# Performance work log

Measured on AMD Instinct MI355X. Metric: run time of the kernel, lower is better.

## Reference

```python
import jax, jax.numpy as jnp
import numpy as np
import math

SR = 44100
N_SAMPLES = 64000
HZ_MAX = 8000.0
LOG10 = math.log(10.0)
# DDSP unit_to_hz with hz_min=0 (hz_to_midi(0) -> 0), hz_max=8000
MIDI_MIN = 0.0
MIDI_MAX = 12.0 * (math.log2(HZ_MAX) - math.log2(440.0)) + 69.0


def scale_function(x):
    # 2 * sigmoid(x)**log(10) + 1e-7
    return 2.0 * jax.nn.sigmoid(x) ** LOG10 + 1e-7


def frequencies_sigmoid(freqs):
    # depth=1: single sigmoid component, log-scale (midi) mapping to [0, 8000] Hz
    unit = jax.nn.sigmoid(freqs)                      # [B, T, K]
    midi = MIDI_MIN + unit * (MIDI_MAX - MIDI_MIN)
    return 440.0 * 2.0 ** ((midi - 69.0) / 12.0)


def remove_above_nyquist(amplitudes, pitch):
    n_harm = amplitudes.shape[-1]
    harmonics = jnp.arange(1, n_harm + 1, dtype=pitch.dtype)
    aa = (pitch * harmonics < SR / 2).astype(pitch.dtype) + 1e-4
    return amplitudes * aa


def upsample_with_windows(x, n_timesteps):
    # x: [B, n_frames, C]; add_endpoint=True
    x = jnp.concatenate([x, x[:, -1:, :]], axis=1)    # [B, F1, C]
    b, f1, c = x.shape
    n_intervals = f1 - 1
    hop = n_timesteps // n_intervals
    win_len = 2 * hop
    # periodic hann window (torch.hann_window default)
    window = (0.5 * (1.0 - jnp.cos(2.0 * jnp.pi * jnp.arange(win_len) / win_len))).astype(x.dtype)
    xw = x.transpose(0, 2, 1)[..., None] * window     # [B, C, F1, 2*hop]
    # overlap-add with frame_step = hop: split each frame into two hop-sized halves
    halves = xw.reshape(b, c, f1, 2, hop)
    out = jnp.zeros((b, c, f1 + 1, hop), x.dtype)
    out = out.at[:, :, :f1].add(halves[:, :, :, 0])
    out = out.at[:, :, 1:].add(halves[:, :, :, 1])
    out = out.reshape(b, c, -1).transpose(0, 2, 1)    # [B, (F1+1)*hop, C]
    return out[:, hop:-hop, :]                        # [B, n_timesteps, C]


def reference(amplitudes, frequencies):
    # get_controls
    amps = scale_function(amplitudes)
    freqs = frequencies_sigmoid(frequencies)
    amps = remove_above_nyquist(amps, freqs)
    # get_signal
    amplitude_envelopes = upsample_with_windows(amps, N_SAMPLES)
    # faithful to source bug: resample_m('linear') returns its input unchanged
    frequency_envelopes = freqs
    return amplitude_envelopes, frequency_envelopes


def setup_inputs() -> dict:
    key = jax.random.key(0)
    k1, k2 = jax.random.split(key)
    amplitudes = jax.random.normal(k1, (8, 250, 100), dtype=jnp.float32)
    frequencies = jax.random.normal(k2, (8, 250, 100), dtype=jnp.float32)
    return {"amplitudes": amplitudes, "frequencies": frequencies}
```

## Files before the change

kernel.cpp:

```cpp
#include <hip/hip_runtime.h>


namespace {
constexpr int kB = 8;
constexpr int kF = 250;
constexpr int kC = 100;
constexpr int kHop = 256;
constexpr int kSamples = 64000;
constexpr int kFreqElems = kB * kF * kC;
constexpr size_t kAmpElems = (size_t)kB * kSamples * kC;
constexpr float kLog10 = 2.302585092994046f;
constexpr float kMidiMax = 119.213094853649121f;
constexpr float kPi = 3.14159265358979323846f;

__device__ __forceinline__ float sigmoidf_(float x) {
    return 1.0f / (1.0f + expf(-x));
}
}

__global__ __launch_bounds__(256) void amp_kernel(
    const float* amp_in,
    const float* frq_in,
    float* amp_out)
{
    const int gm1 = blockIdx.x;
    const int b   = blockIdx.y;
    const int tid = threadIdx.x;

    __shared__ float sAprev[kC];
    __shared__ float sAcur[kC];
    __shared__ float sWin[kHop];

    sWin[tid] = 0.5f * (1.0f - cosf(kPi * (float)tid * (1.0f / 256.0f)));

    if (tid < 2 * kC) {
        const int which = (tid >= kC) ? 1 : 0;
        const int c = which ? (tid - kC) : tid;
        const int frame = which ? min(gm1 + 1, kF - 1) : gm1;
        const int idx = (b * kF + frame) * kC + c;
        const float xa = amp_in[idx];
        const float xf = frq_in[idx];
        const float a  = 2.0f * powf(sigmoidf_(xa), kLog10) + 1e-7f;
        const float f  = 440.0f * exp2f((sigmoidf_(xf) * kMidiMax - 69.0f) * (1.0f / 12.0f));
        const float aa = (f * (float)(c + 1) < 22050.0f) ? (1.0f + 1e-4f) : 1e-4f;
        const float A = a * aa;
        if (which) sAcur[c] = A; else sAprev[c] = A;
    }
    __syncthreads();

    const size_t base = ((size_t)b * kSamples + (size_t)gm1 * kHop) * (size_t)kC;
    for (int k = tid; k < kHop * kC; k += 256) {
        const int q = k / 100;
        const int c = k - q * 100;
        const float wr = sWin[q];
        const float ap = sAprev[c];
        const float ag = sAcur[c];
        amp_out[base + (size_t)k] = fmaf(wr, ag - ap, ap);
    }
}

__global__ __launch_bounds__(256) void freq_kernel(
    const float* frq_in,
    float* frq_out)
{
    const int i = blockIdx.x * 256 + threadIdx.x;
    if (i < kFreqElems) {
        const float xf = frq_in[i];
        frq_out[i] = 440.0f * exp2f((sigmoidf_(xf) * kMidiMax - 69.0f) * (1.0f / 12.0f));
    }
}

extern "C" void kernel_launch(void* const* d_in, const int* in_sizes, int n_in,
                              void* d_out, int out_size, void* d_ws, size_t ws_size,
                              hipStream_t stream) {
    (void)in_sizes; (void)n_in; (void)out_size; (void)d_ws; (void)ws_size;
    const float* amp = (const float*)d_in[0];
    const float* frq = (const float*)d_in[1];
    float* out0 = (float*)d_out;
    float* out1 = out0 + kAmpElems;

    dim3 grid(kF, kB);
    amp_kernel<<<grid, 256, 0, stream>>>(amp, frq, out0);

    const int fblocks = (kFreqElems + 255) / 256;
    freq_kernel<<<fblocks, 256, 0, stream>>>(frq, out1);
}
```

Baseline: 202.2 us.

## Fuse freq output into amp kernel and vectorize envelope stores with nontemporal writes

```diff
diff --git a/kernel.cpp b/kernel.cpp
--- a/kernel.cpp
+++ b/kernel.cpp
@@ -7,28 +7,30 @@
 constexpr int kC = 100;
 constexpr int kHop = 256;
 constexpr int kSamples = 64000;
-constexpr int kFreqElems = kB * kF * kC;
 constexpr size_t kAmpElems = (size_t)kB * kSamples * kC;
 constexpr float kLog10 = 2.302585092994046f;
 constexpr float kMidiMax = 119.213094853649121f;
 constexpr float kPi = 3.14159265358979323846f;
+
+typedef float f32x4 __attribute__((ext_vector_type(4)));
 
 __device__ __forceinline__ float sigmoidf_(float x) {
     return 1.0f / (1.0f + expf(-x));
 }
 }
 
-__global__ __launch_bounds__(256) void amp_kernel(
-    const float* amp_in,
-    const float* frq_in,
-    float* amp_out)
+__global__ __launch_bounds__(256) void synth_kernel(
+    const float* __restrict__ amp_in,
+    const float* __restrict__ frq_in,
+    float* __restrict__ amp_out,
+    float* __restrict__ frq_out)
 {
     const int gm1 = blockIdx.x;
     const int b   = blockIdx.y;
     const int tid = threadIdx.x;
 
-    __shared__ float sAprev[kC];
-    __shared__ float sAcur[kC];
+    __shared__ __align__(16) float sAp[kC];
+    __shared__ __align__(16) float sD[kC];
     __shared__ float sWin[kHop];
 
     sWin[tid] = 0.5f * (1.0f - cosf(kPi * (float)tid * (1.0f / 256.0f)));
@@ -44,29 +46,36 @@
         const float f  = 440.0f * exp2f((sigmoidf_(xf) * kMidiMax - 69.0f) * (1.0f / 12.0f));
         const float aa = (f * (float)(c + 1) < 22050.0f) ? (1.0f + 1e-4f) : 1e-4f;
         const float A = a * aa;
-        if (which) sAcur[c] = A; else sAprev[c] = A;
+        if (which) {
+            sD[c] = A;
+        } else {
+            sAp[c] = A;
+            frq_out[idx] = f;
+        }
     }
     __syncthreads();
+    if (tid < kC) sD[tid] -= sAp[tid];
+    __syncthreads();
 
-    const size_t base = ((size_t)b * kSamples + (size_t)gm1 * kHop) * (size_t)kC;
-    for (int k = tid; k < kHop * kC; k += 256) {
-        const int q = k / 100;
-        const int c = k - q * 100;
-        const float wr = sWin[q];
-        const float ap = sAprev[c];
-        const float ag = sAcur[c];
-        amp_out[base + (size_t)k] = fmaf(wr, ag - ap, ap);
-    }
-}
+    const size_t base4 = (((size_t)b * kSamples + (size_t)gm1 * kHop) * (size_t)kC) / 4;
+    f32x4* __restrict__ out4 = reinterpret_cast<f32x4*>(amp_out) + base4;
+    const f32x4* ap4 = reinterpret_cast<const f32x4*>(sAp);
+    const f32x4* d4  = reinterpret_cast<const f32x4*>(sD);
 
-__global__ __launch_bounds__(256) void freq_kernel(
-    const float* frq_in,
-    float* frq_out)
-{
-    const int i = blockIdx.x * 256 + threadIdx.x;
-    if (i < kFreqElems) {
-        const float xf = frq_in[i];
-        frq_out[i] = 440.0f * exp2f((sigmoidf_(xf) * kMidiMax - 69.0f) * (1.0f / 12.0f));
+#pragma unroll
+    for (int it = 0; it < 25; ++it) {
+        const int fidx = tid + (it << 8);
+        const int q = fidx / 25;
+        const int m = fidx - q * 25;
+        const float w = sWin[q];
+        const f32x4 a = ap4[m];
+        const f32x4 d = d4[m];
+        f32x4 o;
+        o.x = fmaf(w, d.x, a.x);
+        o.y = fmaf(w, d.y, a.y);
+        o.z = fmaf(w, d.z, a.z);
+        o.w = fmaf(w, d.w, a.w);
+        __builtin_nontemporal_store(o, out4 + fidx);
     }
 }
 
@@ -80,8 +89,5 @@
     float* out1 = out0 + kAmpElems;
 
     dim3 grid(kF, kB);
-    amp_kernel<<<grid, 256, 0, stream>>>(amp, frq, out0);
-
-    const int fblocks = (kFreqElems + 255) / 256;
-    freq_kernel<<<fblocks, 256, 0, stream>>>(frq, out1);
+    synth_kernel<<<grid, 256, 0, stream>>>(amp, frq, out0, out1);
 }
```

New measurement: 210.0 us. 3.9% more time.
